# Optimization experiments

Hardware: AMD Instinct MI355X
Metric: run time of the kernel (lower is better)

## Reference

```python
import jax, jax.numpy as jnp
import numpy as np

D_MODEL = 2048
N_HEADS = 16
N_KV = 4
GROUP = N_HEADS // N_KV  # 4
D_K = D_MODEL // N_HEADS  # 128
D_V = D_MODEL // N_KV     # 512
THETA = 10000.0
Q_DIM = N_HEADS * D_K
K_DIM = N_KV * D_K
V_DIM = N_KV * D_V


def _apply_rope(t, sin, cos):
    # t: [B, H, L, D]; sin/cos: [L, D] broadcast over batch/heads
    half = t.shape[-1] // 2
    x1, x2 = t[..., :half], t[..., half:]
    rot = jnp.concatenate([-x2, x1], axis=-1)
    return t * cos + rot * sin


def setup_inputs() -> dict:
    key = jax.random.key(0)
    k1, k2, k3 = jax.random.split(key, 3)
    x = jax.random.normal(k1, (2, 2048, D_MODEL), dtype=jnp.float32)
    # attn_proj: Linear(d_model -> Q_DIM+K_DIM+V_DIM, bias=False); stored as [in, out]
    W_attn = jax.random.normal(k2, (D_MODEL, Q_DIM + K_DIM + V_DIM), dtype=jnp.float32) * 0.02
    # out_proj: Linear(n_heads*d_v -> d_model) with bias
    W_out = jax.random.normal(k3, (N_HEADS * D_V, D_MODEL), dtype=jnp.float32) * 0.02
    b_out = jnp.zeros((D_MODEL,), dtype=jnp.float32)
    return {"x": x, "W_attn": W_attn, "W_out": W_out, "b_out": b_out}


def reference(x, W_attn, W_out, b_out):
    B, L, _ = x.shape
    qkv = x @ W_attn  # [B, L, Q_DIM+K_DIM+V_DIM]
    q = qkv[..., :Q_DIM].reshape(B, L, N_HEADS, D_K).transpose(0, 2, 1, 3)          # [B,H,L,dk]
    k = qkv[..., Q_DIM:Q_DIM + K_DIM].reshape(B, L, N_KV, D_K).transpose(0, 2, 1, 3)  # [B,Hkv,L,dk]
    v = qkv[..., Q_DIM + K_DIM:].reshape(B, L, N_KV, D_V).transpose(0, 2, 1, 3)       # [B,Hkv,L,dv]

    # RoPE (computed in float32, as in source)
    inv_freq = 1.0 / (THETA ** (jnp.arange(0, D_K, 2, dtype=jnp.float32) / D_K))
    freqs = jnp.arange(L, dtype=jnp.float32)[:, None] * inv_freq[None, :]  # [L, dk/2]
    ang = jnp.concatenate([freqs, freqs], axis=-1)                          # [L, dk]
    sin, cos = jnp.sin(ang), jnp.cos(ang)
    q = _apply_rope(q.astype(jnp.float32), sin, cos).astype(x.dtype)
    k = _apply_rope(k.astype(jnp.float32), sin, cos).astype(x.dtype)

    # GQA: repeat_interleave(group, dim=1) is equivalent to grouping q heads as [kv, group]
    qg = q.reshape(B, N_KV, GROUP, L, D_K)
    scores = jnp.einsum('bkgqd,bkld->bkgql', qg, k) / (D_K ** 0.5)  # [B,Hkv,G,L,L]
    probs = jax.nn.softmax(scores, axis=-1)
    ctx = jnp.einsum('bkgql,bkle->bkgqe', probs, v)  # [B,Hkv,G,L,dv]
    ctx = ctx.reshape(B, N_HEADS, L, D_V).transpose(0, 2, 1, 3).reshape(B, L, N_HEADS * D_V)
    return ctx @ W_out + b_out
```

## Files before the change

### kernel.cpp

```cpp
#include <hip/hip_runtime.h>

typedef unsigned short u16;
typedef float f32x4 __attribute__((ext_vector_type(4)));
typedef __bf16 bf16x8 __attribute__((ext_vector_type(8)));

#define DEV static __device__ __forceinline__

DEV u16 f2bf(float f) {
  union { float f; unsigned u; } c; c.f = f;
  unsigned u = c.u;
  u += 0x7fffu + ((u >> 16) & 1u);
  return (u16)(u >> 16);
}
DEV float bf2f(u16 h) {
  union { float f; unsigned u; } c; c.u = ((unsigned)h) << 16;
  return c.f;
}
DEV f32x4 MFMA(bf16x8 a, bf16x8 b, f32x4 c) {
  return __builtin_amdgcn_mfma_f32_16x16x32_bf16(a, b, c, 0, 0, 0);
}
DEV unsigned cvt_pk_bf16(float a, float b) {
  unsigned r;
  asm("v_cvt_pk_bf16_f32 %0, %1, %2" : "=v"(r) : "v"(a), "v"(b));
  return r;
}
DEV void glds16(const void* src, void* lds) {
  __builtin_amdgcn_global_load_lds(
      (__attribute__((address_space(1))) void*)src,
      (__attribute__((address_space(3))) void*)lds, 16, 0, 0);
}


__global__ void rope_tables(float* __restrict__ sinT, float* __restrict__ cosT) {
  int idx = blockIdx.x * 256 + threadIdx.x;
  int l = idx >> 6, i = idx & 63;
  float inv = __expf(-((float)(2 * i) / 128.0f) * 9.210340371976184f);
  float ang = (float)l * inv;
  sinT[idx] = sinf(ang);
  cosT[idx] = cosf(ang);
}

__global__ void cast_f32_bf16(const float* __restrict__ in, u16* __restrict__ out) {
  int i = (blockIdx.x * 256 + threadIdx.x) * 4;
  float4 v = *(const float4*)(in + i);
  ushort4 o;
  o.x = f2bf(v.x); o.y = f2bf(v.y); o.z = f2bf(v.z); o.w = f2bf(v.w);
  *(ushort4*)(out + i) = o;
}

__global__ void transpose_cast(const float* __restrict__ in, u16* __restrict__ out,
                               int R, int C) {
  __shared__ u16 tile[32][33];
  int c0 = blockIdx.x * 32, r0 = blockIdx.y * 32;
  int tx = threadIdx.x, ty = threadIdx.y;
  for (int i = 0; i < 32; i += 8)
    tile[ty + i][tx] = f2bf(in[(size_t)(r0 + ty + i) * C + c0 + tx]);
  __syncthreads();
  for (int i = 0; i < 32; i += 8)
    out[(size_t)(c0 + ty + i) * R + r0 + tx] = tile[tx][ty + i];
}

template <int WRITE_F32>
__global__ __launch_bounds__(256) void gemm_bt(
    const u16* __restrict__ A, const u16* __restrict__ Bt,
    float* __restrict__ Cf, u16* __restrict__ Cb,
    const float* __restrict__ bias, int N, int K) {
  __shared__ __align__(16) u16 lA[128 * 32];
  __shared__ __align__(16) u16 lB[128 * 32];
  const int bn = blockIdx.x, bm = blockIdx.y;
  const int t = threadIdx.x, w = t >> 6, l = t & 63;
  const int wr = w >> 1, wc = w & 1;
  const int lr = l & 15, lg = l >> 4;

  f32x4 zero = {0.f, 0.f, 0.f, 0.f};
  f32x4 acc[4][4];
#pragma unroll
  for (int m = 0; m < 4; ++m)
#pragma unroll
    for (int n = 0; n < 4; ++n) acc[m][n] = zero;

  const int lrow = l >> 2, lslot = l & 3;
  const size_t aBase = (size_t)(bm * 128) * K;
  const size_t bBase = (size_t)(bn * 128) * K;

  for (int k0 = 0; k0 < K; k0 += 32) {
    __syncthreads();
#pragma unroll
    for (int i = 0; i < 2; ++i) {
      int R = w * 16 + i * 64;
      int row = R + lrow;
      int sg = (lslot ^ (row & 3)) * 8;
      glds16(A + aBase + (size_t)row * K + k0 + sg, (u16*)lA + R * 32);
      glds16(Bt + bBase + (size_t)row * K + k0 + sg, (u16*)lB + R * 32);
    }
    __syncthreads();

    bf16x8 af[4], bf[4];
#pragma unroll
    for (int m = 0; m < 4; ++m) {
      int row = wr * 64 + m * 16 + lr;
      int sw = (lg ^ (row & 3)) & 3;
      af[m] = *(const bf16x8*)((char*)lA + row * 64 + sw * 16);
    }
#pragma unroll
    for (int n = 0; n < 4; ++n) {
      int row = wc * 64 + n * 16 + lr;
      int sw = (lg ^ (row & 3)) & 3;
      bf[n] = *(const bf16x8*)((char*)lB + row * 64 + sw * 16);
    }
#pragma unroll
    for (int m = 0; m < 4; ++m)
#pragma unroll
      for (int n = 0; n < 4; ++n)
        acc[m][n] = MFMA(af[m], bf[n], acc[m][n]);
  }

#pragma unroll
  for (int m = 0; m < 4; ++m) {
#pragma unroll
    for (int n = 0; n < 4; ++n) {
      int col = bn * 128 + wc * 64 + n * 16 + lr;
      float bv = WRITE_F32 ? bias[col] : 0.f;
#pragma unroll
      for (int j = 0; j < 4; ++j) {
        size_t rowg = (size_t)(bm * 128 + wr * 64 + m * 16 + lg * 4 + j);
        float v = acc[m][n][j];
        if (WRITE_F32) Cf[rowg * N + col] = v + bv;
        else           Cb[rowg * N + col] = f2bf(v);
      }
    }
  }
}

__global__ void rope_kernel(u16* __restrict__ qkv, const float* __restrict__ sinT,
                            const float* __restrict__ cosT) {
  int idx = blockIdx.x * 256 + threadIdx.x;
  int d = idx & 63;
  int rh = idx >> 6;
  int head = rh % 20;
  int row = rh / 20;
  int lpos = row & 2047;
  int col = head < 16 ? head * 128 : 2048 + (head - 16) * 128;
  float sc = head < 16 ? 0.08838834764831845f : 1.0f;
  u16* p = qkv + (size_t)row * 4608 + col;
  float x1 = bf2f(p[d]), x2 = bf2f(p[d + 64]);
  float c = cosT[lpos * 64 + d], s = sinT[lpos * 64 + d];
  p[d]      = f2bf((x1 * c - x2 * s) * sc);
  p[d + 64] = f2bf((x2 * c + x1 * s) * sc);
}

__global__ void vt_kernel(const u16* __restrict__ qkv, u16* __restrict__ vT) {
  __shared__ u16 tile[32][33];
  int bkv = blockIdx.z;
  int b = bkv >> 2, kv = bkv & 3;
  int e0 = blockIdx.x * 32, l0 = blockIdx.y * 32;
  const u16* src = qkv + (size_t)(b * 2048) * 4608 + 2560 + kv * 512;
  int tx = threadIdx.x, ty = threadIdx.y;
  for (int i = 0; i < 32; i += 8)
    tile[ty + i][tx] = src[(size_t)(l0 + ty + i) * 4608 + e0 + tx];
  __syncthreads();
  u16* dst = vT + (size_t)(bkv * 512) * 2048;
  for (int i = 0; i < 32; i += 8)
    dst[(size_t)(e0 + ty + i) * 2048 + l0 + tx] = tile[tx][ty + i];
}

__global__ __launch_bounds__(512, 2) void attn_kernel(
    const u16* __restrict__ qkv, const u16* __restrict__ vT,
    u16* __restrict__ ctxb) {
  const int wg = blockIdx.x;
  const int pg = wg & 7, qt = wg >> 3;
  const int kvg = pg & 3, b = pg >> 2;
  const int t = threadIdx.x, w = t >> 6, l = t & 63;
  const int lr = l & 15, lg = l >> 4;
  const int h4 = w >> 1, eh = w & 1;
  const int h = kvg * 4 + h4;

  __shared__ __align__(16) u16 lK[32 * 128];
  __shared__ __align__(16) u16 lV[512 * 32];

  f32x4 zero = {0.f, 0.f, 0.f, 0.f};

  bf16x8 qf[2][4];
  const size_t qbase = (size_t)(b * 2048 + qt * 32);
#pragma unroll
  for (int m = 0; m < 2; ++m)
#pragma unroll
    for (int dc = 0; dc < 4; ++dc)
      qf[m][dc] = *(const bf16x8*)(qkv + (qbase + m * 16 + lr) * 4608 + h * 128 + dc * 32 + lg * 8);

  f32x4 acc[2][16];
#pragma unroll
  for (int m = 0; m < 2; ++m)
#pragma unroll
    for (int e = 0; e < 16; ++e) acc[m][e] = zero;
  float m_r[2] = {-1e30f, -1e30f};
  float l_r[2] = {0.f, 0.f};

  const size_t kbase = (size_t)(b * 2048) * 4608 + 2048 + kvg * 128;
  const size_t vbase = (size_t)((b * 4 + kvg) * 512) * 2048;

  const u16* vsrc = vT + vbase + (size_t)(t >> 2) * 2048 + (t & 3) * 8;
  const u16* ksrc = qkv + kbase + (size_t)(t >> 4) * 4608 + (t & 15) * 8;
  char* vdst;
  { int slot = ((t >> 2) & 1) * 4 + (t & 3);
    int sw = slot ^ ((t >> 3) & 7);
    vdst = (char*)lV + (t >> 3) * 128 + sw * 16; }
  char* kdst;
  { int s = t & 15, r7 = (t >> 4) & 7;
    int sw = (s & 8) | ((s ^ r7) & 7);
    kdst = (char*)lK + (t >> 4) * 256 + sw * 16; }

  const int pr7 = (lr >> 1) & 7;
  const int sw1 = (((lr & 1) * 4) + (lg >> 1)) ^ pr7;
  const int sw2 = (((lr & 1) * 4) + 2 + (lg >> 1)) ^ pr7;
  const int vo_base = (eh * 128 + (lr >> 1)) * 128 + (lg & 1) * 8;
  const int vo1 = vo_base + sw1 * 16;
  const int vo2 = vo_base + sw2 * 16;

  bf16x8 vreg[4], kreg;
#pragma unroll
  for (int i = 0; i < 4; ++i) vreg[i] = *(const bf16x8*)(vsrc + (size_t)i * 262144);
  kreg = *(const bf16x8*)(ksrc);

  for (int kv0 = 0; kv0 < 2048; kv0 += 32) {
    __syncthreads();
#pragma unroll
    for (int i = 0; i < 4; ++i) *(bf16x8*)(vdst + i * 8192) = vreg[i];
    *(bf16x8*)(kdst) = kreg;
    if (kv0 + 32 < 2048) {
#pragma unroll
      for (int i = 0; i < 4; ++i)
        vreg[i] = *(const bf16x8*)(vsrc + (kv0 + 32) + (size_t)i * 262144);
      kreg = *(const bf16x8*)(ksrc + (size_t)(kv0 + 32) * 4608);
    }
    __syncthreads();

    f32x4 sT[2][2];
    sT[0][0] = zero; sT[0][1] = zero; sT[1][0] = zero; sT[1][1] = zero;
#pragma unroll
    for (int dc = 0; dc < 4; ++dc) {
      int slot = dc * 4 + lg;
      int sw = (slot & 8) | ((slot ^ (lr & 7)) & 7);
#pragma unroll
      for (int kt = 0; kt < 2; ++kt) {
        bf16x8 kf = *(const bf16x8*)((char*)lK + (kt * 16 + lr) * 256 + sw * 16);
        sT[kt][0] = MFMA(kf, qf[0][dc], sT[kt][0]);
        sT[kt][1] = MFMA(kf, qf[1][dc], sT[kt][1]);
      }
    }

    float rmax[2];
#pragma unroll
    for (int m = 0; m < 2; ++m) {
      float a0 = fmaxf(fmaxf(sT[0][m][0], sT[0][m][1]), fmaxf(sT[0][m][2], sT[0][m][3]));
      float a1 = fmaxf(fmaxf(sT[1][m][0], sT[1][m][1]), fmaxf(sT[1][m][2], sT[1][m][3]));
      float r = fmaxf(a0, a1);
      r = fmaxf(r, __shfl_xor(r, 16));
      r = fmaxf(r, __shfl_xor(r, 32));
      rmax[m] = r;
    }
    bool need = (rmax[0] > m_r[0] + 8.f) || (rmax[1] > m_r[1] + 8.f);
    if (__any(need)) {
#pragma unroll
      for (int m = 0; m < 2; ++m) {
        float mn = fmaxf(m_r[m], rmax[m]);
        float al = __expf(m_r[m] - mn);
        m_r[m] = mn; l_r[m] *= al;
        float alj[4];
#pragma unroll
        for (int j = 0; j < 4; ++j) alj[j] = __shfl(al, lg * 4 + j);
#pragma unroll
        for (int e = 0; e < 16; ++e)
#pragma unroll
          for (int j = 0; j < 4; ++j) acc[m][e][j] *= alj[j];
      }
    }

    bf16x8 pf[2];
#pragma unroll
    for (int m = 0; m < 2; ++m) {
      float p0 = __expf(sT[0][m][0] - m_r[m]), p1 = __expf(sT[0][m][1] - m_r[m]);
      float p2 = __expf(sT[0][m][2] - m_r[m]), p3 = __expf(sT[0][m][3] - m_r[m]);
      float p4 = __expf(sT[1][m][0] - m_r[m]), p5 = __expf(sT[1][m][1] - m_r[m]);
      float p6 = __expf(sT[1][m][2] - m_r[m]), p7 = __expf(sT[1][m][3] - m_r[m]);
      float s = ((p0 + p1) + (p2 + p3)) + ((p4 + p5) + (p6 + p7));
      s += __shfl_xor(s, 16);
      s += __shfl_xor(s, 32);
      l_r[m] += s;
      union { bf16x8 v; unsigned wd[4]; } u;
      u.wd[0] = cvt_pk_bf16(p0, p1);
      u.wd[1] = cvt_pk_bf16(p2, p3);
      u.wd[2] = cvt_pk_bf16(p4, p5);
      u.wd[3] = cvt_pk_bf16(p6, p7);
      pf[m] = u.v;
    }

#pragma unroll
    for (int e = 0; e < 16; ++e) {
      typedef __bf16 bf16x4 __attribute__((ext_vector_type(4)));
      bf16x4 lo = *(const bf16x4*)((char*)lV + vo1 + e * 1024);
      bf16x4 hi = *(const bf16x4*)((char*)lV + vo2 + e * 1024);
      bf16x8 vf = __builtin_shufflevector(lo, hi, 0, 1, 2, 3, 4, 5, 6, 7);
      acc[0][e] = MFMA(pf[0], vf, acc[0][e]);
      acc[1][e] = MFMA(pf[1], vf, acc[1][e]);
    }
  }

#pragma unroll
  for (int m = 0; m < 2; ++m) {
    float linv[4];
#pragma unroll
    for (int j = 0; j < 4; ++j) linv[j] = 1.0f / __shfl(l_r[m], lg * 4 + j);
    const size_t orow0 = qbase + m * 16 + lg * 4;
#pragma unroll
    for (int e = 0; e < 16; ++e)
#pragma unroll
      for (int j = 0; j < 4; ++j)
        ctxb[(orow0 + j) * 8192 + h * 512 + eh * 256 + e * 16 + lr] =
            f2bf(acc[m][e][j] * linv[j]);
  }
}

extern "C" void kernel_launch(void* const* d_in, const int* in_sizes, int n_in,
                              void* d_out, int out_size, void* d_ws, size_t ws_size,
                              hipStream_t stream) {
  const float* x      = (const float*)d_in[0];
  const float* W_attn = (const float*)d_in[1];
  const float* W_out  = (const float*)d_in[2];
  const float* b_out  = (const float*)d_in[3];
  float* out = (float*)d_out;
  char* ws = (char*)d_ws;

  if (ws_size < 158334976u) return;

  float* sinT = (float*)(ws + 0);
  float* cosT = (float*)(ws + 524288);
  u16* xb   = (u16*)(ws + 1048576);
  u16* WbT  = (u16*)(ws + 17825792);
  u16* qkvb = (u16*)(ws + 36700160);
  u16* vT   = (u16*)(ws + 74448896);
  u16* ctxb = (u16*)(ws + 91226112);
  u16* WobT = (u16*)(ws + 1048576);

  rope_tables<<<512, 256, 0, stream>>>(sinT, cosT);
  cast_f32_bf16<<<8192, 256, 0, stream>>>(x, xb);
  transpose_cast<<<dim3(144, 64), dim3(32, 8), 0, stream>>>(W_attn, WbT, 2048, 4608);
  gemm_bt<0><<<dim3(36, 32), 256, 0, stream>>>(xb, WbT, nullptr, qkvb, nullptr, 4608, 2048);
  rope_kernel<<<20480, 256, 0, stream>>>(qkvb, sinT, cosT);
  vt_kernel<<<dim3(16, 64, 8), dim3(32, 8), 0, stream>>>(qkvb, vT);
  attn_kernel<<<512, 512, 0, stream>>>(qkvb, vT, ctxb);
  transpose_cast<<<dim3(64, 256), dim3(32, 8), 0, stream>>>(W_out, WobT, 8192, 2048);
  gemm_bt<1><<<dim3(16, 32), 256, 0, stream>>>(ctxb, WobT, out, nullptr, b_out, 2048, 8192);
}
```

Before: 645.5 us.

## Double-buffer K/V tiles via direct global-to-LDS loads and use exp2 softmax

Replaces the register-staged K/V prefetch with direct global_load_lds into double-buffered LDS tiles, so each iteration needs a single barrier and the loads of the next tile overlap with compute. The V transpose kernel now writes a permuted column order, so each lane reads one 16-byte V fragment from LDS instead of two 8-byte halves. The Q scale folds in log2(e) so the softmax can use the native exp2 instruction, and the rescale threshold is adjusted to match the base-2 domain. This doubles LDS use, which may affect occupancy at two blocks per CU.

```diff
diff --git a/kernel.cpp b/kernel.cpp
--- a/kernel.cpp
+++ b/kernel.cpp
@@ -24,6 +24,7 @@
   asm("v_cvt_pk_bf16_f32 %0, %1, %2" : "=v"(r) : "v"(a), "v"(b));
   return r;
 }
+DEV float ex2(float x) { return __builtin_amdgcn_exp2f(x); }
 DEV void glds16(const void* src, void* lds) {
   __builtin_amdgcn_global_load_lds(
       (__attribute__((address_space(1))) void*)src,
@@ -141,7 +142,7 @@
   int row = rh / 20;
   int lpos = row & 2047;
   int col = head < 16 ? head * 128 : 2048 + (head - 16) * 128;
-  float sc = head < 16 ? 0.08838834764831845f : 1.0f;
+  float sc = head < 16 ? 0.12751743561938476f : 1.0f;
   u16* p = qkv + (size_t)row * 4608 + col;
   float x1 = bf2f(p[d]), x2 = bf2f(p[d + 64]);
   float c = cosT[lpos * 64 + d], s = sinT[lpos * 64 + d];
@@ -160,8 +161,9 @@
     tile[ty + i][tx] = src[(size_t)(l0 + ty + i) * 4608 + e0 + tx];
   __syncthreads();
   u16* dst = vT + (size_t)(bkv * 512) * 2048;
+  int pi = ((tx >> 2) & 3) * 8 + ((tx >> 4) & 1) * 4 + (tx & 3);
   for (int i = 0; i < 32; i += 8)
-    dst[(size_t)(e0 + ty + i) * 2048 + l0 + tx] = tile[tx][ty + i];
+    dst[(size_t)(e0 + ty + i) * 2048 + l0 + pi] = tile[tx][ty + i];
 }
 
 __global__ __launch_bounds__(512, 2) void attn_kernel(
@@ -175,8 +177,8 @@
   const int h4 = w >> 1, eh = w & 1;
   const int h = kvg * 4 + h4;
 
-  __shared__ __align__(16) u16 lK[32 * 128];
-  __shared__ __align__(16) u16 lV[512 * 32];
+  __shared__ __align__(16) u16 lK[2][32 * 128];
+  __shared__ __align__(16) u16 lV[2][256 * 64];
 
   f32x4 zero = {0.f, 0.f, 0.f, 0.f};
 
@@ -199,41 +201,32 @@
   const size_t kbase = (size_t)(b * 2048) * 4608 + 2048 + kvg * 128;
   const size_t vbase = (size_t)((b * 4 + kvg) * 512) * 2048;
 
-  const u16* vsrc = vT + vbase + (size_t)(t >> 2) * 2048 + (t & 3) * 8;
-  const u16* ksrc = qkv + kbase + (size_t)(t >> 4) * 4608 + (t & 15) * 8;
-  char* vdst;
-  { int slot = ((t >> 2) & 1) * 4 + (t & 3);
-    int sw = slot ^ ((t >> 3) & 7);
-    vdst = (char*)lV + (t >> 3) * 128 + sw * 16; }
-  char* kdst;
-  { int s = t & 15, r7 = (t >> 4) & 7;
-    int sw = (s & 8) | ((s ^ r7) & 7);
-    kdst = (char*)lK + (t >> 4) * 256 + sw * 16; }
-
-  const int pr7 = (lr >> 1) & 7;
-  const int sw1 = (((lr & 1) * 4) + (lg >> 1)) ^ pr7;
-  const int sw2 = (((lr & 1) * 4) + 2 + (lg >> 1)) ^ pr7;
-  const int vo_base = (eh * 128 + (lr >> 1)) * 128 + (lg & 1) * 8;
-  const int vo1 = vo_base + sw1 * 16;
-  const int vo2 = vo_base + sw2 * 16;
-
-  bf16x8 vreg[4], kreg;
-#pragma unroll
-  for (int i = 0; i < 4; ++i) vreg[i] = *(const bf16x8*)(vsrc + (size_t)i * 262144);
-  kreg = *(const bf16x8*)(ksrc);
-
-  for (int kv0 = 0; kv0 < 2048; kv0 += 32) {
+  const int krow = t >> 4;
+  const int kp = t & 15;
+  const int ks = (kp & 8) | ((kp ^ (krow & 7)) & 7);
+  const u16* ksrc0 = qkv + kbase + (size_t)krow * 4608 + ks * 8;
+  const int vs = (t & 7) ^ ((t >> 3) & 7);
+  const int ve0 = (t >> 3) * 2 + (vs >> 2);
+  const u16* vsrc0 = vT + vbase + (size_t)ve0 * 2048 + (vs & 3) * 8;
+
+  const int vfoff = (eh * 128 + (lr >> 1)) * 128 +
+                    (((((lr & 1) << 2) | lg) ^ ((lr >> 1) & 7)) << 4);
+
+  auto stage = [&](int bi, int kv0) {
+    glds16(ksrc0 + (size_t)kv0 * 4608, &lK[bi][t * 8]);
+#pragma unroll
+    for (int i = 0; i < 4; ++i)
+      glds16(vsrc0 + kv0 + (size_t)i * 262144, &lV[bi][i * 4096 + t * 8]);
+  };
+
+  stage(0, 0);
+
+  for (int it = 0; it < 64; ++it) {
+    const int cur = it & 1;
     __syncthreads();
-#pragma unroll
-    for (int i = 0; i < 4; ++i) *(bf16x8*)(vdst + i * 8192) = vreg[i];
-    *(bf16x8*)(kdst) = kreg;
-    if (kv0 + 32 < 2048) {
-#pragma unroll
-      for (int i = 0; i < 4; ++i)
-        vreg[i] = *(const bf16x8*)(vsrc + (kv0 + 32) + (size_t)i * 262144);
-      kreg = *(const bf16x8*)(ksrc + (size_t)(kv0 + 32) * 4608);
-    }
-    __syncthreads();
+    if (it + 1 < 64) stage(cur ^ 1, 32 * (it + 1));
+    const char* lKc = (const char*)lK[cur];
+    const char* lVc = (const char*)lV[cur];
 
     f32x4 sT[2][2];
     sT[0][0] = zero; sT[0][1] = zero; sT[1][0] = zero; sT[1][1] = zero;
@@ -243,7 +236,7 @@
       int sw = (slot & 8) | ((slot ^ (lr & 7)) & 7);
 #pragma unroll
       for (int kt = 0; kt < 2; ++kt) {
-        bf16x8 kf = *(const bf16x8*)((char*)lK + (kt * 16 + lr) * 256 + sw * 16);
+        bf16x8 kf = *(const bf16x8*)(lKc + (kt * 16 + lr) * 256 + sw * 16);
         sT[kt][0] = MFMA(kf, qf[0][dc], sT[kt][0]);
         sT[kt][1] = MFMA(kf, qf[1][dc], sT[kt][1]);
       }
@@ -259,12 +252,12 @@
       r = fmaxf(r, __shfl_xor(r, 32));
       rmax[m] = r;
     }
-    bool need = (rmax[0] > m_r[0] + 8.f) || (rmax[1] > m_r[1] + 8.f);
+    bool need = (rmax[0] > m_r[0] + 11.5f) || (rmax[1] > m_r[1] + 11.5f);
     if (__any(need)) {
 #pragma unroll
       for (int m = 0; m < 2; ++m) {
         float mn = fmaxf(m_r[m], rmax[m]);
-        float al = __expf(m_r[m] - mn);
+        float al = ex2(m_r[m] - mn);
         m_r[m] = mn; l_r[m] *= al;
         float alj[4];
 #pragma unroll
@@ -279,10 +272,10 @@
     bf16x8 pf[2];
 #pragma unroll
     for (int m = 0; m < 2; ++m) {
-      float p0 = __expf(sT[0][m][0] - m_r[m]), p1 = __expf(sT[0][m][1] - m_r[m]);
-      float p2 = __expf(sT[0][m][2] - m_r[m]), p3 = __expf(sT[0][m][3] - m_r[m]);
-      float p4 = __expf(sT[1][m][0] - m_r[m]), p5 = __expf(sT[1][m][1] - m_r[m]);
-      float p6 = __expf(sT[1][m][2] - m_r[m]), p7 = __expf(sT[1][m][3] - m_r[m]);
+      float p0 = ex2(sT[0][m][0] - m_r[m]), p1 = ex2(sT[0][m][1] - m_r[m]);
+      float p2 = ex2(sT[0][m][2] - m_r[m]), p3 = ex2(sT[0][m][3] - m_r[m]);
+      float p4 = ex2(sT[1][m][0] - m_r[m]), p5 = ex2(sT[1][m][1] - m_r[m]);
+      float p6 = ex2(sT[1][m][2] - m_r[m]), p7 = ex2(sT[1][m][3] - m_r[m]);
       float s = ((p0 + p1) + (p2 + p3)) + ((p4 + p5) + (p6 + p7));
       s += __shfl_xor(s, 16);
       s += __shfl_xor(s, 32);
@@ -297,10 +290,7 @@
 
 #pragma unroll
     for (int e = 0; e < 16; ++e) {
-      typedef __bf16 bf16x4 __attribute__((ext_vector_type(4)));
-      bf16x4 lo = *(const bf16x4*)((char*)lV + vo1 + e * 1024);
-      bf16x4 hi = *(const bf16x4*)((char*)lV + vo2 + e * 1024);
-      bf16x8 vf = __builtin_shufflevector(lo, hi, 0, 1, 2, 3, 4, 5, 6, 7);
+      bf16x8 vf = *(const bf16x8*)(lVc + vfoff + e * 1024);
       acc[0][e] = MFMA(pf[0], vf, acc[0][e]);
       acc[1][e] = MFMA(pf[1], vf, acc[1][e]);
     }
```

Result: faster. 629.5 us (-2.5%).
